# Performance work log

Hardware: AMD Instinct MI355X
Metric: run time of the kernel (lower is better)

## Reference

```python
import jax, jax.numpy as jnp
import numpy as np
from jax import lax

N_PTS = 500000
CH = 64
GRID = 256
BN_EPS = 1e-5
A = -0.75  # torch bicubic coefficient


def setup_inputs() -> dict:
    key = jax.random.key(0)
    ks = jax.random.split(key, 10)
    coordinates = jax.random.uniform(ks[0], (N_PTS, 3), jnp.float32) * 2.0 - 1.0  # points in [-1,1]^3
    noise = jax.random.normal(ks[1], (3, N_PTS, 2), jnp.float32) * 0.01  # per-plane coord jitter (is_training)
    plane_x = jax.random.normal(ks[2], (1, CH, GRID, GRID), jnp.float32) * 0.001
    plane_y = jax.random.normal(ks[3], (1, CH, GRID, GRID), jnp.float32) * 0.001
    plane_z = jax.random.normal(ks[4], (1, CH, GRID, GRID), jnp.float32) * 0.001
    fan_in = CH * 9
    conv_w = jax.random.uniform(ks[5], (CH, CH, 3, 3), jnp.float32, -1.0, 1.0) / np.sqrt(fan_in)
    conv_b = jax.random.uniform(ks[6], (CH,), jnp.float32, -1.0, 1.0) / np.sqrt(fan_in)
    bn_gamma = jnp.ones((CH,), jnp.float32)
    bn_beta = jnp.zeros((CH,), jnp.float32)
    return {"coordinates": coordinates, "noise": noise, "plane_x": plane_x,
            "plane_y": plane_y, "plane_z": plane_z, "conv_w": conv_w,
            "conv_b": conv_b, "bn_gamma": bn_gamma, "bn_beta": bn_beta}


def res_block(p, conv_w, conv_b, gamma, beta):
    # conv3x3 stride2 pad1 -> BN (batch stats, training mode) -> relu, + avgpool3x3 s2 p1 (count_include_pad)
    y = lax.conv_general_dilated(p, conv_w, (2, 2), [(1, 1), (1, 1)],
                                 dimension_numbers=("NCHW", "OIHW", "NCHW"))
    y = y + conv_b[None, :, None, None]
    mu = jnp.mean(y, axis=(0, 2, 3), keepdims=True)
    var = jnp.var(y, axis=(0, 2, 3), keepdims=True)  # biased, as torch BN uses for normalization
    y = (y - mu) * lax.rsqrt(var + BN_EPS) * gamma[None, :, None, None] + beta[None, :, None, None]
    y = jax.nn.relu(y)
    pooled = lax.reduce_window(p, 0.0, lax.add, (1, 1, 3, 3), (1, 1, 2, 2),
                               [(0, 0), (0, 0), (1, 1), (1, 1)]) / 9.0
    return y + pooled


def cubic_weights(t):
    # torch cubic convolution weights, a=-0.75; t in [0,1). returns (4, M)
    t1 = t + 1.0
    w0 = ((A * t1 - 5 * A) * t1 + 8 * A) * t1 - 4 * A
    w1 = ((A + 2) * t - (A + 3)) * t * t + 1.0
    s = 1.0 - t
    w2 = ((A + 2) * s - (A + 3)) * s * s + 1.0
    w3 = 1.0 - w0 - w1 - w2
    return jnp.stack([w0, w1, w2, w3])


def sample_plane_bicubic(plane, grid):
    # plane: (C,H,W); grid: (M,2) with grid[:,0]->W axis, grid[:,1]->H axis (torch grid_sample layout)
    # bicubic, padding_mode='border', align_corners=True
    C, H, W = plane.shape
    gx = jnp.clip((grid[:, 0] + 1.0) * 0.5 * (W - 1), 0.0, W - 1.0)
    gy = jnp.clip((grid[:, 1] + 1.0) * 0.5 * (H - 1), 0.0, H - 1.0)
    x0f = jnp.floor(gx); y0f = jnp.floor(gy)
    tx = gx - x0f; ty = gy - y0f
    x0 = x0f.astype(jnp.int32); y0 = y0f.astype(jnp.int32)
    wx = cubic_weights(tx)  # (4,M)
    wy = cubic_weights(ty)  # (4,M)
    pl = jnp.transpose(plane, (1, 2, 0))  # (H,W,C)
    out = jnp.zeros((grid.shape[0], C), plane.dtype)
    for i in range(4):  # fixed 4x4 bicubic footprint
        yi = jnp.clip(y0 + (i - 1), 0, H - 1)
        for j in range(4):
            xi = jnp.clip(x0 + (j - 1), 0, W - 1)
            out = out + (wy[i] * wx[j])[:, None] * pl[yi, xi]
    return out  # (M,C)


def reference(coordinates, noise, plane_x, plane_y, plane_z, conv_w, conv_b, bn_gamma, bn_beta):
    bound = 1.0
    c = (coordinates + bound) / (2.0 * bound)  # (N,3) in [0,1] (fed to grid_sample as-is, faithful)
    px = res_block(plane_x, conv_w, conv_b, bn_gamma, bn_beta)[0]  # (C,128,128)
    py = res_block(plane_y, conv_w, conv_b, bn_gamma, bn_beta)[0]
    pz = res_block(plane_z, conv_w, conv_b, bn_gamma, bn_beta)[0]
    xy = sample_plane_bicubic(px, c[:, 0:2] + noise[0])
    yz = sample_plane_bicubic(py, c[:, 1:3] + noise[1])
    xz = sample_plane_bicubic(pz, c[:, 0:3:2] + noise[2])
    return xy + yz + xz  # (N,C)
```

## Files before the change

### kernel.cpp

```cpp
#include <hip/hip_runtime.h>
#include <hip/hip_fp16.h>

#define N_POINTS 500000
#define BN_EPS 1e-5f
#define A_COEF -0.75f

typedef __attribute__((ext_vector_type(8))) short short8;
typedef __attribute__((ext_vector_type(4))) float floatx4;
typedef unsigned short ushort_t;
typedef unsigned int uint_t;
typedef __attribute__((ext_vector_type(4))) uint_t uintx4;

#define WS_WBF_OFF    0
#define WS_CONV_OFF   18432
#define WS_SUM_OFF    (WS_CONV_OFF + 3145728)
#define WS_SUMSQ_OFF  (WS_SUM_OFF + 192)
#define WS_SCALE_OFF  (WS_SUMSQ_OFF + 192)
#define WS_SHIFT_OFF  (WS_SCALE_OFF + 192)
#define WS_PLANES_OFF (WS_SHIFT_OFF + 192)
#define WS_INBF_OFF   (WS_PLANES_OFF + 1572864)

__device__ __forceinline__ ushort_t f2bf(float f) {
  uint_t u = __float_as_uint(f);
  uint_t r = (u + 0x7fffu + ((u >> 16) & 1u)) >> 16;
  return (ushort_t)r;
}
__device__ __forceinline__ float bf2f(ushort_t u) {
  return __uint_as_float(((uint_t)u) << 16);
}

__global__ __launch_bounds__(256) void wprep_kernel(const float* __restrict__ w_in,
                                                    float* __restrict__ ws) {
  int i = blockIdx.x * 256 + threadIdx.x;
  if (i < 36864) {
    int ic = i & 63;
    int oc = (i >> 6) & 63;
    int kk = i >> 12;
    ((ushort_t*)(ws + WS_WBF_OFF))[i] = f2bf(w_in[(oc * 64 + ic) * 9 + kk]);
  }
  if (i < 384) ws[WS_SUM_OFF + i] = 0.0f;
}

__global__ __launch_bounds__(256) void transpose_kernel(const float* __restrict__ p0,
                                                        const float* __restrict__ p1,
                                                        const float* __restrict__ p2,
                                                        float* __restrict__ ws) {
  __shared__ float tile[64][65];
  const int xt = blockIdx.x, y = blockIdx.y, pl = blockIdx.z;
  const float* src = (pl == 0) ? p0 : ((pl == 1) ? p1 : p2);
  ushort_t* dst = (ushort_t*)(ws + WS_INBF_OFF) + pl * (256 * 256 * 64);
  const int t = threadIdx.x;
  const int x0 = xt * 64;
  for (int i = t; i < 4096; i += 256) {
    int c = i >> 6, x = i & 63;
    tile[x][c] = src[(c * 256 + y) * 256 + x0 + x];
  }
  __syncthreads();
  uint_t* du = (uint_t*)dst;
  for (int i = t; i < 2048; i += 256) {
    int x = i >> 5, cp = (i & 31) * 2;
    uint_t lo = f2bf(tile[x][cp]);
    uint_t hi = f2bf(tile[x][cp + 1]);
    du[((y * 256 + x0 + x) * 64 + cp) >> 1] = (hi << 16) | lo;
  }
}

__global__ __launch_bounds__(256) void conv_mfma_kernel(const float* __restrict__ ws_r,
                                                        float* __restrict__ ws) {
  const int xh = blockIdx.x, oy = blockIdx.y, pz = blockIdx.z;
  const int t = threadIdx.x;
  const int wv = t >> 6, lane = t & 63;
  const int mn = lane & 15;
  const int kg = lane >> 4;
  const int x0w = xh * 64 + wv * 16;

  const ushort_t* inb = (const ushort_t*)(ws_r + WS_INBF_OFF) + pz * (256 * 256 * 64);
  const ushort_t* wbf = (const ushort_t*)(ws_r + WS_WBF_OFF);

  floatx4 acc[4] = {{0.f,0.f,0.f,0.f},{0.f,0.f,0.f,0.f},{0.f,0.f,0.f,0.f},{0.f,0.f,0.f,0.f}};

  for (int ky = 0; ky < 3; ky++) {
    int y = 2 * oy - 1 + ky;
    if (y < 0) continue;
    const ushort_t* rowp = inb + y * (256 * 64);
    for (int kx = 0; kx < 3; kx++) {
      int xm = 2 * (x0w + mn) - 1 + kx;
      bool vx = xm >= 0;
      int xc = vx ? xm : 0;
      const ushort_t* abase = rowp + xc * 64 + kg * 8;
      const ushort_t* wbase = wbf + ((ky * 3 + kx) * 64 + mn) * 64 + kg * 8;
#pragma unroll
      for (int kc = 0; kc < 2; kc++) {
        union { int4 i4; short8 s8; } au;
        au.i4 = *reinterpret_cast<const int4*>(abase + kc * 32);
        if (!vx) au.i4 = make_int4(0, 0, 0, 0);
#pragma unroll
        for (int nt = 0; nt < 4; nt++) {
          union { int4 i4; short8 s8; } bu;
          bu.i4 = *reinterpret_cast<const int4*>(wbase + nt * 1024 + kc * 32);
          acc[nt] = __builtin_amdgcn_mfma_f32_16x16x32_bf16(au.s8, bu.s8, acc[nt], 0, 0, 0);
        }
      }
    }
  }
  float* cout = ws + WS_CONV_OFF + ((pz * 128 + oy) * 128 + x0w) * 64;
#pragma unroll
  for (int nt = 0; nt < 4; nt++) {
#pragma unroll
    for (int r = 0; r < 4; r++) {
      cout[(kg * 4 + r) * 64 + nt * 16 + mn] = acc[nt][r];
    }
  }
}

__global__ __launch_bounds__(256) void stats_kernel(float* __restrict__ ws) {
  const int b = blockIdx.x;
  const int plane = b >> 6, chunk = b & 63;
  const int t = threadIdx.x;
  const int c = t & 63, g = t >> 6;
  const float* base = ws + WS_CONV_OFF + plane * (16384 * 64);
  float s = 0.0f, s2 = 0.0f;
  const int row0 = chunk * 256 + g * 64;
  for (int i = 0; i < 64; i++) {
    float v = base[(row0 + i) * 64 + c];
    s += v;
    s2 = fmaf(v, v, s2);
  }
  __shared__ float rs[256], rs2[256];
  rs[t] = s; rs2[t] = s2;
  __syncthreads();
  if (t < 64) {
    s = rs[t] + rs[t + 64] + rs[t + 128] + rs[t + 192];
    s2 = rs2[t] + rs2[t + 64] + rs2[t + 128] + rs2[t + 192];
    atomicAdd(&ws[WS_SUM_OFF + plane * 64 + c], s);
    atomicAdd(&ws[WS_SUMSQ_OFF + plane * 64 + c], s2);
  }
}

__global__ void finalize_kernel(const float* __restrict__ gamma,
                                const float* __restrict__ beta,
                                float* __restrict__ ws) {
  int i = threadIdx.x;
  if (i < 192) {
    int c = i & 63;
    float mu = ws[WS_SUM_OFF + i] * (1.0f / 16384.0f);
    float var = ws[WS_SUMSQ_OFF + i] * (1.0f / 16384.0f) - mu * mu;
    var = fmaxf(var, 0.0f);
    float rstd = 1.0f / sqrtf(var + BN_EPS);
    float sc = gamma[c] * rstd;
    ws[WS_SCALE_OFF + i] = sc;
    ws[WS_SHIFT_OFF + i] = beta[c] - mu * sc;
  }
}

__global__ __launch_bounds__(256) void apply_kernel(float* __restrict__ ws,
                                                    __half* __restrict__ planes) {
  int idx = blockIdx.x * 256 + threadIdx.x;
  int g = idx & 7;
  int p = (idx >> 3) & 16383;
  int pl = idx >> 17;
  int oy = p >> 7, ox = p & 127;
  int cb = g * 8;

  const float* conv = ws + WS_CONV_OFF;
  float4 a0 = *reinterpret_cast<const float4*>(conv + (size_t)idx * 8);
  float4 a1 = *reinterpret_cast<const float4*>(conv + (size_t)idx * 8 + 4);

  float sc[8], sh[8];
#pragma unroll
  for (int k = 0; k < 8; k++) {
    sc[k] = ws[WS_SCALE_OFF + pl * 64 + cb + k];
    sh[k] = ws[WS_SHIFT_OFF + pl * 64 + cb + k];
  }

  const ushort_t* inb = (const ushort_t*)(ws + WS_INBF_OFF) + pl * (256 * 256 * 64);
  float ps[8];
#pragma unroll
  for (int k = 0; k < 8; k++) ps[k] = 0.0f;
#pragma unroll
  for (int r = 0; r < 3; r++) {
    int yy = 2 * oy - 1 + r;
    if (yy < 0) continue;
#pragma unroll
    for (int s = 0; s < 3; s++) {
      int xx = 2 * ox - 1 + s;
      if (xx < 0) continue;
      union { int4 i4; ushort_t u[8]; } ub;
      ub.i4 = *reinterpret_cast<const int4*>(inb + (yy * 256 + xx) * 64 + cb);
#pragma unroll
      for (int k = 0; k < 8; k++) ps[k] += bf2f(ub.u[k]);
    }
  }

  float v[8] = {a0.x, a0.y, a0.z, a0.w, a1.x, a1.y, a1.z, a1.w};
  union { int4 i4; __half h[8]; } ob;
#pragma unroll
  for (int k = 0; k < 8; k++) {
    float r = fmaxf(fmaf(v[k], sc[k], sh[k]), 0.0f) + ps[k] * (1.0f / 9.0f);
    ob.h[k] = __float2half(r);
  }
  *reinterpret_cast<int4*>(planes + (size_t)idx * 8) = ob.i4;
}

__device__ __forceinline__ void cubic_w(float t, float w[4]) {
  float t1 = t + 1.0f;
  w[0] = ((A_COEF * t1 - 5.0f * A_COEF) * t1 + 8.0f * A_COEF) * t1 - 4.0f * A_COEF;
  w[1] = ((A_COEF + 2.0f) * t - (A_COEF + 3.0f)) * t * t + 1.0f;
  float s = 1.0f - t;
  w[2] = ((A_COEF + 2.0f) * s - (A_COEF + 3.0f)) * s * s + 1.0f;
  w[3] = 1.0f - w[0] - w[1] - w[2];
}

__device__ __forceinline__ void gl8(uintx4& q0, uintx4& q1, uintx4& q2, uintx4& q3,
                                    uintx4& q4, uintx4& q5, uintx4& q6, uintx4& q7,
                                    uint_t o0, uint_t o1, uint_t o2, uint_t o3,
                                    uint_t o4, uint_t o5, uint_t o6, uint_t o7,
                                    const __half* base) {
  asm volatile(
      "global_load_dwordx4 %0, %8, %16\n\t"
      "global_load_dwordx4 %1, %9, %16\n\t"
      "global_load_dwordx4 %2, %10, %16\n\t"
      "global_load_dwordx4 %3, %11, %16\n\t"
      "global_load_dwordx4 %4, %12, %16\n\t"
      "global_load_dwordx4 %5, %13, %16\n\t"
      "global_load_dwordx4 %6, %14, %16\n\t"
      "global_load_dwordx4 %7, %15, %16"
      : "=&v"(q0), "=&v"(q1), "=&v"(q2), "=&v"(q3),
        "=&v"(q4), "=&v"(q5), "=&v"(q6), "=&v"(q7)
      : "v"(o0), "v"(o1), "v"(o2), "v"(o3),
        "v"(o4), "v"(o5), "v"(o6), "v"(o7),
        "s"(base));
}

__device__ __forceinline__ void fma_mix_tap(float& a0, float& a1, float& a2, float& a3,
                                            float& a4, float& a5, float& a6, float& a7,
                                            uint_t qx, uint_t qy, uint_t qz, uint_t qw,
                                            float w) {
  asm("v_fma_mix_f32 %0, %8, %12, %0 op_sel:[0,0,0] op_sel_hi:[1,0,0]\n\t"
      "v_fma_mix_f32 %1, %8, %12, %1 op_sel:[1,0,0] op_sel_hi:[1,0,0]\n\t"
      "v_fma_mix_f32 %2, %9, %12, %2 op_sel:[0,0,0] op_sel_hi:[1,0,0]\n\t"
      "v_fma_mix_f32 %3, %9, %12, %3 op_sel:[1,0,0] op_sel_hi:[1,0,0]\n\t"
      "v_fma_mix_f32 %4, %10, %12, %4 op_sel:[0,0,0] op_sel_hi:[1,0,0]\n\t"
      "v_fma_mix_f32 %5, %10, %12, %5 op_sel:[1,0,0] op_sel_hi:[1,0,0]\n\t"
      "v_fma_mix_f32 %6, %11, %12, %6 op_sel:[0,0,0] op_sel_hi:[1,0,0]\n\t"
      "v_fma_mix_f32 %7, %11, %12, %7 op_sel:[1,0,0] op_sel_hi:[1,0,0]"
      : "+v"(a0), "+v"(a1), "+v"(a2), "+v"(a3),
        "+v"(a4), "+v"(a5), "+v"(a6), "+v"(a7)
      : "v"(qx), "v"(qy), "v"(qz), "v"(qw), "v"(w));
}

__global__ __launch_bounds__(256) void sample_kernel(const float* __restrict__ coords,
                                                     const float* __restrict__ noise,
                                                     const __half* __restrict__ planes,
                                                     float* __restrict__ out) {
  const int t = threadIdx.x;
  const int wv = t >> 6, lane = t & 63;
  const int g = lane >> 3, l = lane & 7;
  const int n = blockIdx.x * 32 + wv * 8 + g;

  const float c0 = (coords[n * 3 + 0] + 1.0f) * 0.5f;
  const float c1 = (coords[n * 3 + 1] + 1.0f) * 0.5f;
  const float c2 = (coords[n * 3 + 2] + 1.0f) * 0.5f;

  float wxA[3][4], wyA[3][4];
  int ixA[3], iyA[3];
#pragma unroll
  for (int p = 0; p < 3; p++) {
    float u = (p == 1) ? c1 : c0;
    float v = (p == 0) ? c1 : c2;
    u += noise[(p * N_POINTS + n) * 2 + 0];
    v += noise[(p * N_POINTS + n) * 2 + 1];
    float gx = fminf(fmaxf(fmaf(u, 63.5f, 63.5f), 0.0f), 127.0f);
    float gy = fminf(fmaxf(fmaf(v, 63.5f, 63.5f), 0.0f), 127.0f);
    float x0f = floorf(gx), y0f = floorf(gy);
    cubic_w(gx - x0f, wxA[p]);
    cubic_w(gy - y0f, wyA[p]);
    ixA[p] = (int)x0f;
    iyA[p] = (int)y0f;
  }

  float a0 = 0.f, a1 = 0.f, a2 = 0.f, a3 = 0.f;
  float a4 = 0.f, a5 = 0.f, a6 = 0.f, a7 = 0.f;

#pragma unroll
  for (int p = 0; p < 3; p++) {
    const int ix = ixA[p], iy = iyA[p];
    const int rb = p * (128 * 128 * 64) + l * 8;
    int ro[4], xo[4];
#pragma unroll
    for (int i = 0; i < 4; i++) ro[i] = rb + min(max(iy - 1 + i, 0), 127) * (128 * 64);
#pragma unroll
    for (int j = 0; j < 4; j++) xo[j] = min(max(ix - 1 + j, 0), 127) * 64;

    uint_t off[16];
#pragma unroll
    for (int i = 0; i < 4; i++)
#pragma unroll
      for (int j = 0; j < 4; j++) off[i * 4 + j] = (uint_t)(ro[i] + xo[j]) * 2u;

    uintx4 q0, q1, q2, q3, q4, q5, q6, q7, q8, q9, qa, qb, qc, qd, qe, qf;
    gl8(q0, q1, q2, q3, q4, q5, q6, q7,
        off[0], off[1], off[2], off[3], off[4], off[5], off[6], off[7], planes);
    gl8(q8, q9, qa, qb, qc, qd, qe, qf,
        off[8], off[9], off[10], off[11], off[12], off[13], off[14], off[15], planes);

    asm volatile("s_waitcnt vmcnt(8)");
    __builtin_amdgcn_sched_barrier(0);
    fma_mix_tap(a0,a1,a2,a3,a4,a5,a6,a7, q0.x,q0.y,q0.z,q0.w, wyA[p][0]*wxA[p][0]);
    fma_mix_tap(a0,a1,a2,a3,a4,a5,a6,a7, q1.x,q1.y,q1.z,q1.w, wyA[p][0]*wxA[p][1]);
    fma_mix_tap(a0,a1,a2,a3,a4,a5,a6,a7, q2.x,q2.y,q2.z,q2.w, wyA[p][0]*wxA[p][2]);
    fma_mix_tap(a0,a1,a2,a3,a4,a5,a6,a7, q3.x,q3.y,q3.z,q3.w, wyA[p][0]*wxA[p][3]);
    fma_mix_tap(a0,a1,a2,a3,a4,a5,a6,a7, q4.x,q4.y,q4.z,q4.w, wyA[p][1]*wxA[p][0]);
    fma_mix_tap(a0,a1,a2,a3,a4,a5,a6,a7, q5.x,q5.y,q5.z,q5.w, wyA[p][1]*wxA[p][1]);
    fma_mix_tap(a0,a1,a2,a3,a4,a5,a6,a7, q6.x,q6.y,q6.z,q6.w, wyA[p][1]*wxA[p][2]);
    fma_mix_tap(a0,a1,a2,a3,a4,a5,a6,a7, q7.x,q7.y,q7.z,q7.w, wyA[p][1]*wxA[p][3]);

    asm volatile("s_waitcnt vmcnt(0)");
    __builtin_amdgcn_sched_barrier(0);
    fma_mix_tap(a0,a1,a2,a3,a4,a5,a6,a7, q8.x,q8.y,q8.z,q8.w, wyA[p][2]*wxA[p][0]);
    fma_mix_tap(a0,a1,a2,a3,a4,a5,a6,a7, q9.x,q9.y,q9.z,q9.w, wyA[p][2]*wxA[p][1]);
    fma_mix_tap(a0,a1,a2,a3,a4,a5,a6,a7, qa.x,qa.y,qa.z,qa.w, wyA[p][2]*wxA[p][2]);
    fma_mix_tap(a0,a1,a2,a3,a4,a5,a6,a7, qb.x,qb.y,qb.z,qb.w, wyA[p][2]*wxA[p][3]);
    fma_mix_tap(a0,a1,a2,a3,a4,a5,a6,a7, qc.x,qc.y,qc.z,qc.w, wyA[p][3]*wxA[p][0]);
    fma_mix_tap(a0,a1,a2,a3,a4,a5,a6,a7, qd.x,qd.y,qd.z,qd.w, wyA[p][3]*wxA[p][1]);
    fma_mix_tap(a0,a1,a2,a3,a4,a5,a6,a7, qe.x,qe.y,qe.z,qe.w, wyA[p][3]*wxA[p][2]);
    fma_mix_tap(a0,a1,a2,a3,a4,a5,a6,a7, qf.x,qf.y,qf.z,qf.w, wyA[p][3]*wxA[p][3]);
  }

  float* op = out + (size_t)n * 64 + l * 8;
  *reinterpret_cast<float4*>(op)     = make_float4(a0, a1, a2, a3);
  *reinterpret_cast<float4*>(op + 4) = make_float4(a4, a5, a6, a7);
}

extern "C" void kernel_launch(void* const* d_in, const int* in_sizes, int n_in,
                              void* d_out, int out_size, void* d_ws, size_t ws_size,
                              hipStream_t stream) {
  const float* coords = (const float*)d_in[0];
  const float* noise  = (const float*)d_in[1];
  const float* px     = (const float*)d_in[2];
  const float* py     = (const float*)d_in[3];
  const float* pz     = (const float*)d_in[4];
  const float* conv_w = (const float*)d_in[5];
  const float* gamma  = (const float*)d_in[7];
  const float* beta   = (const float*)d_in[8];
  float* out = (float*)d_out;
  float* ws = (float*)d_ws;
  __half* planes = (__half*)(ws + WS_PLANES_OFF);

  wprep_kernel<<<144, 256, 0, stream>>>(conv_w, ws);
  transpose_kernel<<<dim3(4, 256, 3), 256, 0, stream>>>(px, py, pz, ws);
  conv_mfma_kernel<<<dim3(2, 128, 3), 256, 0, stream>>>(ws, ws);
  stats_kernel<<<192, 256, 0, stream>>>(ws);
  finalize_kernel<<<1, 256, 0, stream>>>(gamma, beta, ws);
  apply_kernel<<<1536, 256, 0, stream>>>(ws, planes);
  sample_kernel<<<15625, 256, 0, stream>>>(coords, noise, planes, out);
}
```

Baseline: 350.2 us.

## Software-pipeline plane gathers so next plane's loads overlap current FMAs

The sampling kernel now issues the 16 gather loads for the next plane before consuming the second half of the current plane's taps, using explicit vmcnt waits to keep up to 32 loads in flight. Before, each plane's loads were issued only after the previous plane's FMAs had fully drained. The aim is to hide memory latency across planes, at the cost of holding up to two planes of loaded fragments in registers at once. That higher register pressure may reduce occupancy.

Measured after the change: 356.8 us. Within noise of the previous version (+1.9%).

```diff
diff --git a/kernel.cpp b/kernel.cpp
--- a/kernel.cpp
+++ b/kernel.cpp
@@ -249,6 +249,32 @@
       : "v"(qx), "v"(qy), "v"(qz), "v"(qw), "v"(w));
 }
 
+#define VMW8()  do { asm volatile("s_waitcnt vmcnt(8)");  __builtin_amdgcn_sched_barrier(0); } while (0)
+#define VMW16() do { asm volatile("s_waitcnt vmcnt(16)"); __builtin_amdgcn_sched_barrier(0); } while (0)
+#define VMW0()  do { asm volatile("s_waitcnt vmcnt(0)");  __builtin_amdgcn_sched_barrier(0); } while (0)
+
+__device__ __forceinline__ void mk_offs(int rb, int ix, int iy, uint_t off[16]) {
+  int ro[4], xo[4];
+#pragma unroll
+  for (int i = 0; i < 4; i++) ro[i] = rb + min(max(iy - 1 + i, 0), 127) * (128 * 64);
+#pragma unroll
+  for (int j = 0; j < 4; j++) xo[j] = min(max(ix - 1 + j, 0), 127) * 64;
+#pragma unroll
+  for (int i = 0; i < 4; i++)
+#pragma unroll
+    for (int j = 0; j < 4; j++) off[i * 4 + j] = (uint_t)(ro[i] + xo[j]) * 2u;
+}
+
+#define CONS8(Q0,Q1,Q2,Q3,Q4,Q5,Q6,Q7, P, I0)                                         \
+  fma_mix_tap(a0,a1,a2,a3,a4,a5,a6,a7, Q0.x,Q0.y,Q0.z,Q0.w, wyA[P][I0]*wxA[P][0]);    \
+  fma_mix_tap(a0,a1,a2,a3,a4,a5,a6,a7, Q1.x,Q1.y,Q1.z,Q1.w, wyA[P][I0]*wxA[P][1]);    \
+  fma_mix_tap(a0,a1,a2,a3,a4,a5,a6,a7, Q2.x,Q2.y,Q2.z,Q2.w, wyA[P][I0]*wxA[P][2]);    \
+  fma_mix_tap(a0,a1,a2,a3,a4,a5,a6,a7, Q3.x,Q3.y,Q3.z,Q3.w, wyA[P][I0]*wxA[P][3]);    \
+  fma_mix_tap(a0,a1,a2,a3,a4,a5,a6,a7, Q4.x,Q4.y,Q4.z,Q4.w, wyA[P][I0+1]*wxA[P][0]);  \
+  fma_mix_tap(a0,a1,a2,a3,a4,a5,a6,a7, Q5.x,Q5.y,Q5.z,Q5.w, wyA[P][I0+1]*wxA[P][1]);  \
+  fma_mix_tap(a0,a1,a2,a3,a4,a5,a6,a7, Q6.x,Q6.y,Q6.z,Q6.w, wyA[P][I0+1]*wxA[P][2]);  \
+  fma_mix_tap(a0,a1,a2,a3,a4,a5,a6,a7, Q7.x,Q7.y,Q7.z,Q7.w, wyA[P][I0+1]*wxA[P][3]);
+
 __global__ __launch_bounds__(256) void sample_kernel(const float* __restrict__ coords,
                                                      const float* __restrict__ noise,
                                                      const __half* __restrict__ planes,
@@ -282,50 +308,41 @@
   float a0 = 0.f, a1 = 0.f, a2 = 0.f, a3 = 0.f;
   float a4 = 0.f, a5 = 0.f, a6 = 0.f, a7 = 0.f;
 
-#pragma unroll
-  for (int p = 0; p < 3; p++) {
-    const int ix = ixA[p], iy = iyA[p];
-    const int rb = p * (128 * 128 * 64) + l * 8;
-    int ro[4], xo[4];
-#pragma unroll
-    for (int i = 0; i < 4; i++) ro[i] = rb + min(max(iy - 1 + i, 0), 127) * (128 * 64);
-#pragma unroll
-    for (int j = 0; j < 4; j++) xo[j] = min(max(ix - 1 + j, 0), 127) * 64;
-
-    uint_t off[16];
-#pragma unroll
-    for (int i = 0; i < 4; i++)
-#pragma unroll
-      for (int j = 0; j < 4; j++) off[i * 4 + j] = (uint_t)(ro[i] + xo[j]) * 2u;
-
-    uintx4 q0, q1, q2, q3, q4, q5, q6, q7, q8, q9, qa, qb, qc, qd, qe, qf;
-    gl8(q0, q1, q2, q3, q4, q5, q6, q7,
-        off[0], off[1], off[2], off[3], off[4], off[5], off[6], off[7], planes);
-    gl8(q8, q9, qa, qb, qc, qd, qe, qf,
-        off[8], off[9], off[10], off[11], off[12], off[13], off[14], off[15], planes);
-
-    asm volatile("s_waitcnt vmcnt(8)");
-    __builtin_amdgcn_sched_barrier(0);
-    fma_mix_tap(a0,a1,a2,a3,a4,a5,a6,a7, q0.x,q0.y,q0.z,q0.w, wyA[p][0]*wxA[p][0]);
-    fma_mix_tap(a0,a1,a2,a3,a4,a5,a6,a7, q1.x,q1.y,q1.z,q1.w, wyA[p][0]*wxA[p][1]);
-    fma_mix_tap(a0,a1,a2,a3,a4,a5,a6,a7, q2.x,q2.y,q2.z,q2.w, wyA[p][0]*wxA[p][2]);
-    fma_mix_tap(a0,a1,a2,a3,a4,a5,a6,a7, q3.x,q3.y,q3.z,q3.w, wyA[p][0]*wxA[p][3]);
-    fma_mix_tap(a0,a1,a2,a3,a4,a5,a6,a7, q4.x,q4.y,q4.z,q4.w, wyA[p][1]*wxA[p][0]);
-    fma_mix_tap(a0,a1,a2,a3,a4,a5,a6,a7, q5.x,q5.y,q5.z,q5.w, wyA[p][1]*wxA[p][1]);
-    fma_mix_tap(a0,a1,a2,a3,a4,a5,a6,a7, q6.x,q6.y,q6.z,q6.w, wyA[p][1]*wxA[p][2]);
-    fma_mix_tap(a0,a1,a2,a3,a4,a5,a6,a7, q7.x,q7.y,q7.z,q7.w, wyA[p][1]*wxA[p][3]);
-
-    asm volatile("s_waitcnt vmcnt(0)");
-    __builtin_amdgcn_sched_barrier(0);
-    fma_mix_tap(a0,a1,a2,a3,a4,a5,a6,a7, q8.x,q8.y,q8.z,q8.w, wyA[p][2]*wxA[p][0]);
-    fma_mix_tap(a0,a1,a2,a3,a4,a5,a6,a7, q9.x,q9.y,q9.z,q9.w, wyA[p][2]*wxA[p][1]);
-    fma_mix_tap(a0,a1,a2,a3,a4,a5,a6,a7, qa.x,qa.y,qa.z,qa.w, wyA[p][2]*wxA[p][2]);
-    fma_mix_tap(a0,a1,a2,a3,a4,a5,a6,a7, qb.x,qb.y,qb.z,qb.w, wyA[p][2]*wxA[p][3]);
-    fma_mix_tap(a0,a1,a2,a3,a4,a5,a6,a7, qc.x,qc.y,qc.z,qc.w, wyA[p][3]*wxA[p][0]);
-    fma_mix_tap(a0,a1,a2,a3,a4,a5,a6,a7, qd.x,qd.y,qd.z,qd.w, wyA[p][3]*wxA[p][1]);
-    fma_mix_tap(a0,a1,a2,a3,a4,a5,a6,a7, qe.x,qe.y,qe.z,qe.w, wyA[p][3]*wxA[p][2]);
-    fma_mix_tap(a0,a1,a2,a3,a4,a5,a6,a7, qf.x,qf.y,qf.z,qf.w, wyA[p][3]*wxA[p][3]);
-  }
+  const int lb = l * 8;
+  uint_t offa[16], offb[16], offc[16];
+  mk_offs(0 * (128 * 128 * 64) + lb, ixA[0], iyA[0], offa);
+
+  uintx4 A0,A1,A2,A3,A4,A5,A6,A7,A8,A9,Aa,Ab,Ac,Ad,Ae,Af;
+  uintx4 B0,B1,B2,B3,B4,B5,B6,B7,B8,B9,Ba,Bb,Bc,Bd,Be,Bf;
+  uintx4 C0,C1,C2,C3,C4,C5,C6,C7,C8,C9,Ca,Cb,Cc,Cd,Ce,Cf;
+
+  gl8(A0,A1,A2,A3,A4,A5,A6,A7, offa[0],offa[1],offa[2],offa[3],offa[4],offa[5],offa[6],offa[7], planes);
+  gl8(A8,A9,Aa,Ab,Ac,Ad,Ae,Af, offa[8],offa[9],offa[10],offa[11],offa[12],offa[13],offa[14],offa[15], planes);
+
+  mk_offs(1 * (128 * 128 * 64) + lb, ixA[1], iyA[1], offb);
+  mk_offs(2 * (128 * 128 * 64) + lb, ixA[2], iyA[2], offc);
+
+  VMW8();
+  CONS8(A0,A1,A2,A3,A4,A5,A6,A7, 0, 0)
+  gl8(B0,B1,B2,B3,B4,B5,B6,B7, offb[0],offb[1],offb[2],offb[3],offb[4],offb[5],offb[6],offb[7], planes);
+  gl8(B8,B9,Ba,Bb,Bc,Bd,Be,Bf, offb[8],offb[9],offb[10],offb[11],offb[12],offb[13],offb[14],offb[15], planes);
+
+  VMW16();
+  CONS8(A8,A9,Aa,Ab,Ac,Ad,Ae,Af, 0, 2)
+
+  VMW8();
+  CONS8(B0,B1,B2,B3,B4,B5,B6,B7, 1, 0)
+  gl8(C0,C1,C2,C3,C4,C5,C6,C7, offc[0],offc[1],offc[2],offc[3],offc[4],offc[5],offc[6],offc[7], planes);
+  gl8(C8,C9,Ca,Cb,Cc,Cd,Ce,Cf, offc[8],offc[9],offc[10],offc[11],offc[12],offc[13],offc[14],offc[15], planes);
+
+  VMW16();
+  CONS8(B8,B9,Ba,Bb,Bc,Bd,Be,Bf, 1, 2)
+
+  VMW8();
+  CONS8(C0,C1,C2,C3,C4,C5,C6,C7, 2, 0)
+
+  VMW0();
+  CONS8(C8,C9,Ca,Cb,Cc,Cd,Ce,Cf, 2, 2)
 
   float* op = out + (size_t)n * 64 + l * 8;
   *reinterpret_cast<float4*>(op)     = make_float4(a0, a1, a2, a3);
```

## Fuse BN statistics into conv epilogue and finalize into apply kernel

Applied to the files above, without the earlier changes.

The conv MFMA kernel now reduces per-channel sum and sum-of-squares from its accumulators with wave shuffles and atomically adds them to the workspace. The apply kernel computes scale and shift directly from those sums, gamma and beta. Together these remove the separate stats and finalize launches and a full re-read of the conv output buffer. In exchange, the conv epilogue does more global atomics with contention on 128 addresses per plane, and every apply thread recomputes the BN scale and shift.

New measurement: 383.0 us. 9.4% more time.

```diff
diff --git a/kernel.cpp b/kernel.cpp
--- a/kernel.cpp
+++ b/kernel.cpp
@@ -111,49 +111,30 @@
       cout[(kg * 4 + r) * 64 + nt * 16 + mn] = acc[nt][r];
     }
   }
-}
-
-__global__ __launch_bounds__(256) void stats_kernel(float* __restrict__ ws) {
-  const int b = blockIdx.x;
-  const int plane = b >> 6, chunk = b & 63;
-  const int t = threadIdx.x;
-  const int c = t & 63, g = t >> 6;
-  const float* base = ws + WS_CONV_OFF + plane * (16384 * 64);
-  float s = 0.0f, s2 = 0.0f;
-  const int row0 = chunk * 256 + g * 64;
-  for (int i = 0; i < 64; i++) {
-    float v = base[(row0 + i) * 64 + c];
-    s += v;
-    s2 = fmaf(v, v, s2);
-  }
-  __shared__ float rs[256], rs2[256];
-  rs[t] = s; rs2[t] = s2;
-  __syncthreads();
-  if (t < 64) {
-    s = rs[t] + rs[t + 64] + rs[t + 128] + rs[t + 192];
-    s2 = rs2[t] + rs2[t + 64] + rs2[t + 128] + rs2[t + 192];
-    atomicAdd(&ws[WS_SUM_OFF + plane * 64 + c], s);
-    atomicAdd(&ws[WS_SUMSQ_OFF + plane * 64 + c], s2);
-  }
-}
-
-__global__ void finalize_kernel(const float* __restrict__ gamma,
-                                const float* __restrict__ beta,
-                                float* __restrict__ ws) {
-  int i = threadIdx.x;
-  if (i < 192) {
-    int c = i & 63;
-    float mu = ws[WS_SUM_OFF + i] * (1.0f / 16384.0f);
-    float var = ws[WS_SUMSQ_OFF + i] * (1.0f / 16384.0f) - mu * mu;
-    var = fmaxf(var, 0.0f);
-    float rstd = 1.0f / sqrtf(var + BN_EPS);
-    float sc = gamma[c] * rstd;
-    ws[WS_SCALE_OFF + i] = sc;
-    ws[WS_SHIFT_OFF + i] = beta[c] - mu * sc;
+
+  float* sums  = ws + WS_SUM_OFF + pz * 64;
+  float* sumsq = ws + WS_SUMSQ_OFF + pz * 64;
+#pragma unroll
+  for (int nt = 0; nt < 4; nt++) {
+    float s = 0.f, s2 = 0.f;
+#pragma unroll
+    for (int r = 0; r < 4; r++) {
+      float v = acc[nt][r];
+      s += v;
+      s2 = fmaf(v, v, s2);
+    }
+    s += __shfl_xor(s, 16, 64);  s2 += __shfl_xor(s2, 16, 64);
+    s += __shfl_xor(s, 32, 64);  s2 += __shfl_xor(s2, 32, 64);
+    if (kg == 0) {
+      atomicAdd(&sums[nt * 16 + mn], s);
+      atomicAdd(&sumsq[nt * 16 + mn], s2);
+    }
   }
 }
 
 __global__ __launch_bounds__(256) void apply_kernel(float* __restrict__ ws,
+                                                    const float* __restrict__ gamma,
+                                                    const float* __restrict__ beta,
                                                     __half* __restrict__ planes) {
   int idx = blockIdx.x * 256 + threadIdx.x;
   int g = idx & 7;
@@ -169,8 +150,14 @@
   float sc[8], sh[8];
 #pragma unroll
   for (int k = 0; k < 8; k++) {
-    sc[k] = ws[WS_SCALE_OFF + pl * 64 + cb + k];
-    sh[k] = ws[WS_SHIFT_OFF + pl * 64 + cb + k];
+    int c = cb + k;
+    float mu = ws[WS_SUM_OFF + pl * 64 + c] * (1.0f / 16384.0f);
+    float var = ws[WS_SUMSQ_OFF + pl * 64 + c] * (1.0f / 16384.0f) - mu * mu;
+    var = fmaxf(var, 0.0f);
+    float rstd = 1.0f / sqrtf(var + BN_EPS);
+    float s = gamma[c] * rstd;
+    sc[k] = s;
+    sh[k] = beta[c] - mu * s;
   }
 
   const ushort_t* inb = (const ushort_t*)(ws + WS_INBF_OFF) + pl * (256 * 256 * 64);
@@ -350,8 +337,6 @@
   wprep_kernel<<<144, 256, 0, stream>>>(conv_w, ws);
   transpose_kernel<<<dim3(4, 256, 3), 256, 0, stream>>>(px, py, pz, ws);
   conv_mfma_kernel<<<dim3(2, 128, 3), 256, 0, stream>>>(ws, ws);
-  stats_kernel<<<192, 256, 0, stream>>>(ws);
-  finalize_kernel<<<1, 256, 0, stream>>>(gamma, beta, ws);
-  apply_kernel<<<1536, 256, 0, stream>>>(ws, planes);
+  apply_kernel<<<1536, 256, 0, stream>>>(ws, gamma, beta, planes);
   sample_kernel<<<15625, 256, 0, stream>>>(coords, noise, planes, out);
 }
```
